# Optimization experiments

Hardware: AMD Instinct MI355X
Metric: run time of the kernel (lower is better)

The kernel has to match this reference:

```python
import jax, jax.numpy as jnp
import numpy as np

EPS = 1e-10


def setup_inputs() -> dict:
    key = jax.random.key(0)
    k1, k2 = jax.random.split(key)
    x = jax.random.normal(k1, (64, 512, 256), dtype=jnp.float32)          # (N, code_dim, T)
    codebooks = jax.random.normal(k2, (6, 1024, 512), dtype=jnp.float32)  # (Q, nb_code, code_dim)
    return {"x": x, "codebooks": codebooks}


def _quantize_layer(x_flat, cb):
    # x_flat: (NT, D), cb: (C, D)
    dist = (jnp.sum(x_flat * x_flat, axis=-1, keepdims=True)
            - 2.0 * (x_flat @ cb.T)
            + jnp.sum(cb * cb, axis=-1))          # (NT, C)
    idx = jnp.argmin(dist, axis=-1)               # (NT,)
    x_d = cb[idx]                                 # gather, (NT, D)
    return idx, x_d


def reference(x, codebooks):
    N, D, T = x.shape
    Q, C, _ = codebooks.shape
    NT = N * T

    residual = x
    quantized_out = jnp.zeros_like(x)
    all_indices, losses, perps = [], [], []

    for q in range(Q):  # fixed small number of sequential quantizer stages
        cb = codebooks[q]
        # preprocess: (N, D, T) -> (NT, D)
        x_flat = residual.transpose(0, 2, 1).reshape(NT, D)
        idx, x_d = _quantize_layer(x_flat, cb)

        # commitment loss (codebook side detached; EMA-trained codebook)
        commit_loss = jnp.mean((x_flat - jax.lax.stop_gradient(x_d)) ** 2)

        # perplexity of code usage
        probs = jnp.zeros((C,), dtype=x.dtype).at[idx].add(1.0) / NT
        perplexity = jnp.exp(-jnp.sum(probs * jnp.log(probs + EPS)))

        # straight-through estimator, back to (N, D, T)
        quantized = x_flat + jax.lax.stop_gradient(x_d - x_flat)
        quantized = quantized.reshape(N, T, D).transpose(0, 2, 1)

        residual = residual - jax.lax.stop_gradient(quantized)
        quantized_out = quantized_out + quantized

        all_indices.append(idx.reshape(N, T))
        losses.append(commit_loss)
        perps.append(perplexity)

    all_indices = jnp.stack(all_indices, axis=-1)      # (N, T, Q)
    mean_loss = sum(losses) / Q
    mean_perplexity = sum(perps) / Q
    return quantized_out, all_indices, mean_loss, mean_perplexity
```

## Files before the change

### kernel.cpp

```cpp
#include <hip/hip_runtime.h>
#include <hip/hip_fp16.h>
#include <hip/hip_bf16.h>
#include <stdint.h>


#define NTROWS 16384
#define DDIM   512
#define CCODES 1024
#define QSTAGE 6

#define OFF_R      ((size_t)0)
#define OFF_RBF    ((size_t)33554432)
#define OFF_CBBF   ((size_t)50331648)
#define OFF_CAND   ((size_t)56623104)
#define OFF_CBSQ   ((size_t)58720256)
#define OFF_HIST   ((size_t)58744832)
#define OFF_LOSS   ((size_t)58769408)
#define WS_END     ((size_t)58775552)

#define OUT_IDX_OFF  ((size_t)8388608)
#define OUT_SCAL_OFF ((size_t)8486912)

typedef __attribute__((ext_vector_type(8))) short short8;
typedef __attribute__((ext_vector_type(8))) unsigned short ushort8v;
typedef __attribute__((ext_vector_type(4))) float f32x4;

__device__ __forceinline__ unsigned short f2bf(float f) {
    uint32_t u = __float_as_uint(f);
    uint32_t r = (u + 0x7fffu + ((u >> 16) & 1u)) >> 16;
    return (unsigned short)r;
}
__device__ __forceinline__ uint32_t fkey(float f) {
    uint32_t u = __float_as_uint(f);
    return u ^ ((uint32_t)((int32_t)u >> 31) | 0x80000000u);
}
__device__ __forceinline__ float funkey(uint32_t k) {
    uint32_t u = (k & 0x80000000u) ? (k ^ 0x80000000u) : ~k;
    return __uint_as_float(u);
}
__device__ __forceinline__ uint32_t umin32(uint32_t a, uint32_t b) { return a < b ? a : b; }
__device__ __forceinline__ uint32_t umax32(uint32_t a, uint32_t b) { return a > b ? a : b; }
__device__ __forceinline__ float wave_sum(float v) {
    for (int m = 32; m; m >>= 1) v += __shfl_xor(v, m, 64);
    return v;
}
__device__ __forceinline__ uint32_t wave_min_u32(uint32_t v) {
    for (int m = 32; m; m >>= 1) v = umin32(v, (uint32_t)__shfl_xor((int)v, m, 64));
    return v;
}
__device__ __forceinline__ void async_load16(const void* g, void* l) {
    __builtin_amdgcn_global_load_lds(
        (__attribute__((address_space(1))) void*)(void*)g,
        (__attribute__((address_space(3))) void*)l, 16, 0, 0);
}

__global__ __launch_bounds__(256) void prep_kernel(
    const float* __restrict__ x, const float* __restrict__ cb,
    float* __restrict__ r, unsigned short* __restrict__ rbf,
    unsigned short* __restrict__ cbbf, float* __restrict__ cbsq,
    unsigned int* __restrict__ hist, float* __restrict__ loss_bins)
{
    __shared__ float tile[32][33];
    if (blockIdx.x < 1536) {
        const int wave = threadIdx.x >> 6, lane = threadIdx.x & 63;
        const int row = blockIdx.x * 4 + wave;
        const float* p = cb + (size_t)row * DDIM;
        unsigned short* pb = cbbf + (size_t)row * DDIM;
        float s = 0.f;
#pragma unroll
        for (int t = 0; t < 8; ++t) {
            float v = p[lane + 64 * t];
            pb[lane + 64 * t] = f2bf(v);
            s += v * v;
        }
        s = wave_sum(s);
        if (lane == 0) cbsq[row] = s;
        if (blockIdx.x == 0) {
            for (int i = threadIdx.x; i < QSTAGE * CCODES; i += 256) hist[i] = 0u;
            for (int i = threadIdx.x; i < QSTAGE * 256; i += 256) loss_bins[i] = 0.f;
        }
    } else {
        const int bidx = blockIdx.x - 1536;
        const int d0 = (bidx & 15) * 32;
        const int t0 = ((bidx >> 4) & 7) * 32;
        const int n  = bidx >> 7;
        const int tx = threadIdx.x & 31, ty = threadIdx.x >> 5;
        const float* xp = x + (size_t)n * (DDIM * 256);
#pragma unroll
        for (int s = 0; s < 4; ++s) {
            int dd = ty + s * 8;
            tile[dd][tx] = xp[(size_t)(d0 + dd) * 256 + t0 + tx];
        }
        __syncthreads();
#pragma unroll
        for (int s = 0; s < 4; ++s) {
            int tt = ty + s * 8;
            float v = tile[tx][tt];
            size_t off = (size_t)(n * 256 + t0 + tt) * DDIM + d0 + tx;
            r[off] = v;
            rbf[off] = f2bf(v);
        }
    }
}

#define GBK 32
__global__ __launch_bounds__(512, 2) void gemm_dist_kernel(
    const unsigned short* __restrict__ Abf,
    const unsigned short* __restrict__ Bbf,
    const float* __restrict__ cbsq,
    uint32_t* __restrict__ cand)
{
    __shared__ __align__(16) unsigned short lA[4][256][GBK];
    __shared__ __align__(16) unsigned short lB[4][256][GBK];
    const int tid = threadIdx.x;
    const int wave = tid >> 6, lane = tid & 63;
    const int quad = lane >> 4, l15 = lane & 15;
    const int tm = blockIdx.x, tn = blockIdx.y;
    const int wm = wave >> 2, wn = wave & 3;

    f32x4 acc[8][4];
#pragma unroll
    for (int i = 0; i < 8; ++i)
#pragma unroll
        for (int j = 0; j < 4; ++j) acc[i][j] = (f32x4){0.f, 0.f, 0.f, 0.f};

    const int srow = wave * 32 + (lane >> 2);
    const int gch  = (lane & 3) ^ ((lane >> 3) & 3);
    const unsigned short* gA0 = Abf + ((size_t)tm * 256 + srow) * DDIM + gch * 8;
    const unsigned short* gA1 = gA0 + 16 * DDIM;
    const unsigned short* gB0 = Bbf + ((size_t)tn * 256 + srow) * DDIM + gch * 8;
    const unsigned short* gB1 = gB0 + 16 * DDIM;
    const int dro0 = wave * 32, dro1 = wave * 32 + 16;

#pragma unroll
    for (int st = 0; st < 3; ++st) {
        const size_t ko = (size_t)st * GBK;
        async_load16(gA0 + ko, &lA[st][dro0][0] + lane * 8);
        async_load16(gA1 + ko, &lA[st][dro1][0] + lane * 8);
        async_load16(gB0 + ko, &lB[st][dro0][0] + lane * 8);
        async_load16(gB1 + ko, &lB[st][dro1][0] + lane * 8);
    }
    asm volatile("s_waitcnt vmcnt(8)" ::: "memory");
    __builtin_amdgcn_s_barrier();

    const int cq = (quad ^ ((l15 >> 1) & 3)) * 8;

#pragma unroll
    for (int kt = 0; kt < 16; ++kt) {
        const int buf = kt & 3;
        const int sb  = (kt + 3) & 3;
        const size_t ko = (size_t)(kt + 3) * GBK;

        short8 afA[4], bfr[4];
#pragma unroll
        for (int i = 0; i < 4; ++i)
            afA[i] = *(const short8*)&lA[buf][wm * 128 + i * 16 + l15][cq];
#pragma unroll
        for (int j = 0; j < 4; ++j)
            bfr[j] = *(const short8*)&lB[buf][wn * 64 + j * 16 + l15][cq];
        if (kt <= 12) {
            async_load16(gA0 + ko, &lA[sb][dro0][0] + lane * 8);
            async_load16(gA1 + ko, &lA[sb][dro1][0] + lane * 8);
        }
        __builtin_amdgcn_s_barrier();
        asm volatile("s_waitcnt lgkmcnt(0)" ::: "memory");
        __builtin_amdgcn_sched_barrier(0);
        __builtin_amdgcn_s_setprio(1);
#pragma unroll
        for (int i = 0; i < 4; ++i)
#pragma unroll
            for (int j = 0; j < 4; ++j)
                acc[i][j] = __builtin_amdgcn_mfma_f32_16x16x32_bf16(
                    afA[i], bfr[j], acc[i][j], 0, 0, 0);
        __builtin_amdgcn_s_setprio(0);
        __builtin_amdgcn_s_barrier();

        short8 afB[4];
#pragma unroll
        for (int i = 0; i < 4; ++i)
            afB[i] = *(const short8*)&lA[buf][wm * 128 + (i + 4) * 16 + l15][cq];
        if (kt <= 12) {
            async_load16(gB0 + ko, &lB[sb][dro0][0] + lane * 8);
            async_load16(gB1 + ko, &lB[sb][dro1][0] + lane * 8);
        }
        __builtin_amdgcn_s_barrier();
        asm volatile("s_waitcnt lgkmcnt(0)" ::: "memory");
        __builtin_amdgcn_sched_barrier(0);
        __builtin_amdgcn_s_setprio(1);
#pragma unroll
        for (int i = 0; i < 4; ++i)
#pragma unroll
            for (int j = 0; j < 4; ++j)
                acc[i + 4][j] = __builtin_amdgcn_mfma_f32_16x16x32_bf16(
                    afB[i], bfr[j], acc[i + 4][j], 0, 0, 0);
        __builtin_amdgcn_s_setprio(0);

        if (kt <= 12)      asm volatile("s_waitcnt vmcnt(8)" ::: "memory");
        else if (kt == 13) asm volatile("s_waitcnt vmcnt(4)" ::: "memory");
        else if (kt == 14) asm volatile("s_waitcnt vmcnt(0)" ::: "memory");
        if (kt < 15) __builtin_amdgcn_s_barrier();
    }

    const int rowq = tm * 256 + wm * 128 + quad * 4;
    const int colb = tn * 256 + wn * 64 + l15;
    const int g    = tn * 4 + wn;
    float cbs[4];
#pragma unroll
    for (int j = 0; j < 4; ++j) cbs[j] = cbsq[colb + j * 16];
#pragma unroll
    for (int i = 0; i < 8; ++i) {
#pragma unroll
        for (int reg = 0; reg < 4; ++reg) {
            const int row = rowq + i * 16 + reg;
            uint32_t k[4];
#pragma unroll
            for (int j = 0; j < 4; ++j) {
                float dv = cbs[j] - 2.0f * acc[i][j][reg];
                k[j] = (fkey(dv) & ~1023u) | (uint32_t)(colb + j * 16);
            }
            uint32_t m01 = umin32(k[0], k[1]), M01 = umax32(k[0], k[1]);
            uint32_t m23 = umin32(k[2], k[3]), M23 = umax32(k[2], k[3]);
            uint32_t k1 = umin32(m01, m23);
            uint32_t k2 = umin32(umax32(m01, m23), umin32(M01, M23));
#pragma unroll
            for (int m = 1; m < 16; m <<= 1) {
                uint32_t o1 = (uint32_t)__shfl_xor((int)k1, m, 64);
                uint32_t o2 = (uint32_t)__shfl_xor((int)k2, m, 64);
                uint32_t n1 = umin32(k1, o1);
                uint32_t n2 = umin32(umax32(k1, o1), umin32(k2, o2));
                k1 = n1; k2 = n2;
            }
            if (l15 == 0)
                *(uint2*)&cand[((size_t)row * 16 + g) * 2] = make_uint2(k1, k2);
        }
    }
}

#define MARGIN 8.0f
__global__ __launch_bounds__(256, 4) void refine_kernel(
    float* __restrict__ r, unsigned short* __restrict__ rbf,
    const float* __restrict__ cbq, const float* __restrict__ cbsqq,
    const uint32_t* __restrict__ cand,
    float* __restrict__ out_idx, unsigned int* __restrict__ histq,
    float* __restrict__ loss_bins, int q, int write_bf)
{
    const int wave = threadIdx.x >> 6, lane = threadIdx.x & 63;
    const int nt0 = (blockIdx.x * 4 + wave) * 4;

    float4 ra[4], rb[4];
    uint32_t key[4];
#pragma unroll
    for (int i = 0; i < 4; ++i) {
        const float4* r4 = (const float4*)(r + (size_t)(nt0 + i) * DDIM);
        ra[i] = r4[lane * 2];
        rb[i] = r4[lane * 2 + 1];
    }
#pragma unroll
    for (int i = 0; i < 4; ++i) {
        key[i] = 0xFFFFFFFFu;
        if (lane < 32) key[i] = cand[(size_t)(nt0 + i) * 32 + lane];
    }

    uint32_t kmin[4];
#pragma unroll
    for (int i = 0; i < 4; ++i) kmin[i] = key[i];
    for (int m = 32; m; m >>= 1) {
#pragma unroll
        for (int i = 0; i < 4; ++i)
            kmin[i] = umin32(kmin[i], (uint32_t)__shfl_xor((int)kmin[i], m, 64));
    }

    float sx[4];
#pragma unroll
    for (int i = 0; i < 4; ++i)
        sx[i] = ra[i].x * ra[i].x + ra[i].y * ra[i].y + ra[i].z * ra[i].z + ra[i].w * ra[i].w
              + rb[i].x * rb[i].x + rb[i].y * rb[i].y + rb[i].z * rb[i].z + rb[i].w * rb[i].w;
    for (int m = 32; m; m >>= 1) {
#pragma unroll
        for (int i = 0; i < 4; ++i) sx[i] += __shfl_xor(sx[i], m, 64);
    }

    unsigned long long mask[4];
#pragma unroll
    for (int i = 0; i < 4; ++i) {
        const float thr = funkey(kmin[i] & ~1023u) + MARGIN;
        mask[i] = __ballot(lane < 32 && funkey(key[i] & ~1023u) <= thr);
    }

    float best[4] = {1e30f, 1e30f, 1e30f, 1e30f};
    int bestc[4] = {CCODES, CCODES, CCODES, CCODES};

    while (mask[0] | mask[1] | mask[2] | mask[3]) {
        bool act[4]; int src[4], cc[4];
#pragma unroll
        for (int i = 0; i < 4; ++i) {
            act[i] = (mask[i] != 0ull);
            src[i] = act[i] ? (__ffsll(mask[i]) - 1) : 0;
            if (act[i]) mask[i] &= mask[i] - 1;
            cc[i] = __shfl((int)(key[i] & 1023u), src[i], 64);
        }
        float4 ca[4], cbb[4];
#pragma unroll
        for (int i = 0; i < 4; ++i) {
            const float4* crow = (const float4*)(cbq + (size_t)cc[i] * DDIM);
            ca[i]  = crow[lane * 2];
            cbb[i] = crow[lane * 2 + 1];
        }
        float d[4];
#pragma unroll
        for (int i = 0; i < 4; ++i)
            d[i] = ra[i].x * ca[i].x + ra[i].y * ca[i].y + ra[i].z * ca[i].z + ra[i].w * ca[i].w
                 + rb[i].x * cbb[i].x + rb[i].y * cbb[i].y + rb[i].z * cbb[i].z + rb[i].w * cbb[i].w;
        for (int m = 32; m; m >>= 1) {
#pragma unroll
            for (int i = 0; i < 4; ++i) d[i] += __shfl_xor(d[i], m, 64);
        }
#pragma unroll
        for (int i = 0; i < 4; ++i) {
            if (act[i]) {
                const float de = (sx[i] - 2.0f * d[i]) + cbsqq[cc[i]];
                if (de < best[i] || (de == best[i] && cc[i] < bestc[i])) {
                    best[i] = de; bestc[i] = cc[i];
                }
            }
        }
    }

#pragma unroll
    for (int i = 0; i < 4; ++i) {
        const float4* cbest = (const float4*)(cbq + (size_t)bestc[i] * DDIM);
        float4 ba = cbest[lane * 2], bb = cbest[lane * 2 + 1];
        float4 na = make_float4(ra[i].x - ba.x, ra[i].y - ba.y,
                                ra[i].z - ba.z, ra[i].w - ba.w);
        float4 nb = make_float4(rb[i].x - bb.x, rb[i].y - bb.y,
                                rb[i].z - bb.z, rb[i].w - bb.w);
        float4* rw = (float4*)(r + (size_t)(nt0 + i) * DDIM);
        rw[lane * 2] = na; rw[lane * 2 + 1] = nb;
        if (write_bf) {
            ushort8v pk8;
            pk8[0] = f2bf(na.x); pk8[1] = f2bf(na.y);
            pk8[2] = f2bf(na.z); pk8[3] = f2bf(na.w);
            pk8[4] = f2bf(nb.x); pk8[5] = f2bf(nb.y);
            pk8[6] = f2bf(nb.z); pk8[7] = f2bf(nb.w);
            *(ushort8v*)(rbf + (size_t)(nt0 + i) * DDIM + lane * 8) = pk8;
        }
        if (lane == 0) {
            out_idx[(size_t)(nt0 + i) * QSTAGE + q] = (float)bestc[i];
            atomicAdd(&histq[bestc[i]], 1u);
            atomicAdd(&loss_bins[q * 256 + ((nt0 + i) & 255)], best[i]);
        }
    }
}

__global__ __launch_bounds__(256) void final_kernel(
    const float* __restrict__ x, const float* __restrict__ r,
    float* __restrict__ out,
    const unsigned int* __restrict__ hist, const float* __restrict__ loss_bins,
    float* __restrict__ out2)
{
    __shared__ float tile[32][33];
    __shared__ float red[4];
    __shared__ float perp_acc;
    const int tid = threadIdx.x, wave = tid >> 6, lane = tid & 63;

    if (blockIdx.x < 8192) {
        const int bidx = blockIdx.x;
        const int d0 = (bidx & 15) * 32;
        const int t0 = ((bidx >> 4) & 7) * 32;
        const int n  = bidx >> 7;
        const int tx = tid & 31, ty = tid >> 5;
#pragma unroll
        for (int s = 0; s < 4; ++s) {
            int tt = ty + s * 8;
            tile[tt][tx] = r[(size_t)(n * 256 + t0 + tt) * DDIM + d0 + tx];
        }
        __syncthreads();
        const float* xp = x + (size_t)n * (DDIM * 256);
        float* op = out + (size_t)n * (DDIM * 256);
#pragma unroll
        for (int s = 0; s < 4; ++s) {
            int dd = ty + s * 8;
            size_t off = (size_t)(d0 + dd) * 256 + t0 + tx;
            op[off] = xp[off] - tile[tx][dd];
        }
        return;
    }

    if (tid == 0) perp_acc = 0.f;
    __syncthreads();
    for (int q = 0; q < QSTAGE; ++q) {
        float s = 0.f;
        for (int c = tid; c < CCODES; c += 256) {
            float p = (float)hist[q * CCODES + c] * (1.0f / (float)NTROWS);
            s += p * logf(p + 1e-10f);
        }
        s = wave_sum(s);
        if (lane == 0) red[wave] = s;
        __syncthreads();
        if (tid == 0) {
            float tot = red[0] + red[1] + red[2] + red[3];
            perp_acc += expf(-tot);
        }
        __syncthreads();
    }
    float ls = 0.f;
    for (int i = tid; i < QSTAGE * 256; i += 256) ls += loss_bins[i];
    ls = wave_sum(ls);
    if (lane == 0) red[wave] = ls;
    __syncthreads();
    if (tid == 0) {
        float lsum = red[0] + red[1] + red[2] + red[3];
        out2[0] = (lsum / (float)QSTAGE) / ((float)NTROWS * (float)DDIM);
        out2[1] = perp_acc / (float)QSTAGE;
    }
}

extern "C" void kernel_launch(void* const* d_in, const int* in_sizes, int n_in,
                              void* d_out, int out_size, void* d_ws, size_t ws_size,
                              hipStream_t stream)
{
    const float* x  = (const float*)d_in[0];
    const float* cb = (const float*)d_in[1];
    float* out = (float*)d_out;
    char* ws = (char*)d_ws;

    float*          r      = (float*)(ws + OFF_R);
    unsigned short* rbf    = (unsigned short*)(ws + OFF_RBF);
    unsigned short* cbbf   = (unsigned short*)(ws + OFF_CBBF);
    uint32_t*       cand   = (uint32_t*)(ws + OFF_CAND);
    float*          cbsq   = (float*)(ws + OFF_CBSQ);
    unsigned int*   hist   = (unsigned int*)(ws + OFF_HIST);
    float*          lbins  = (float*)(ws + OFF_LOSS);

    prep_kernel<<<9728, 256, 0, stream>>>(x, cb, r, rbf, cbbf, cbsq, hist, lbins);

    for (int q = 0; q < QSTAGE; ++q) {
        const size_t cboff = (size_t)q * CCODES * DDIM;
        gemm_dist_kernel<<<dim3(64, 4), 512, 0, stream>>>(
            rbf, cbbf + cboff, cbsq + q * CCODES, cand);
        refine_kernel<<<1024, 256, 0, stream>>>(
            r, rbf, cb + cboff, cbsq + q * CCODES, cand,
            out + OUT_IDX_OFF, hist + q * CCODES, lbins,
            q, (q < QSTAGE - 1) ? 1 : 0);
    }

    final_kernel<<<8193, 256, 0, stream>>>(x, r, out, hist, lbins,
                                           out + OUT_SCAL_OFF);
}
```

Baseline: 492.5 us.

## Fuse all quantizer stages into one persistent kernel with register-resident residual

Replaces the per-stage GEMM and refine kernel pair (twelve launches) with a single kernel. Each block owns 64 rows, keeps their residual in registers across all six stages, converts it to bf16 straight into LDS, streams codebook tiles, and keeps candidates in LDS instead of global memory. This removes the global round trips for the bf16 residual, the candidate buffer and the fp32 residual between stages, along with the launch overheads. In exchange only 256 blocks of 64 rows run, so there is much less A-tile reuse: every block re-streams the full bf16 codebook for each stage, and occupancy is low.

```diff
diff --git a/kernel.cpp b/kernel.cpp
--- a/kernel.cpp
+++ b/kernel.cpp
@@ -10,13 +10,10 @@
 #define QSTAGE 6
 
 #define OFF_R      ((size_t)0)
-#define OFF_RBF    ((size_t)33554432)
 #define OFF_CBBF   ((size_t)50331648)
-#define OFF_CAND   ((size_t)56623104)
 #define OFF_CBSQ   ((size_t)58720256)
 #define OFF_HIST   ((size_t)58744832)
 #define OFF_LOSS   ((size_t)58769408)
-#define WS_END     ((size_t)58775552)
 
 #define OUT_IDX_OFF  ((size_t)8388608)
 #define OUT_SCAL_OFF ((size_t)8486912)
@@ -44,10 +41,6 @@
     for (int m = 32; m; m >>= 1) v += __shfl_xor(v, m, 64);
     return v;
 }
-__device__ __forceinline__ uint32_t wave_min_u32(uint32_t v) {
-    for (int m = 32; m; m >>= 1) v = umin32(v, (uint32_t)__shfl_xor((int)v, m, 64));
-    return v;
-}
 __device__ __forceinline__ void async_load16(const void* g, void* l) {
     __builtin_amdgcn_global_load_lds(
         (__attribute__((address_space(1))) void*)(void*)g,
@@ -56,7 +49,7 @@
 
 __global__ __launch_bounds__(256) void prep_kernel(
     const float* __restrict__ x, const float* __restrict__ cb,
-    float* __restrict__ r, unsigned short* __restrict__ rbf,
+    float* __restrict__ r,
     unsigned short* __restrict__ cbbf, float* __restrict__ cbsq,
     unsigned int* __restrict__ hist, float* __restrict__ loss_bins)
 {
@@ -95,260 +88,238 @@
 #pragma unroll
         for (int s = 0; s < 4; ++s) {
             int tt = ty + s * 8;
-            float v = tile[tx][tt];
-            size_t off = (size_t)(n * 256 + t0 + tt) * DDIM + d0 + tx;
-            r[off] = v;
-            rbf[off] = f2bf(v);
-        }
-    }
-}
-
-#define GBK 32
-__global__ __launch_bounds__(512, 2) void gemm_dist_kernel(
-    const unsigned short* __restrict__ Abf,
-    const unsigned short* __restrict__ Bbf,
+            r[(size_t)(n * 256 + t0 + tt) * DDIM + d0 + tx] = tile[tx][tt];
+        }
+    }
+}
+
+#define MARGIN 8.0f
+__global__ __launch_bounds__(512, 2) void fused_vq_kernel(
+    float* __restrict__ r,
+    const unsigned short* __restrict__ cbbf,
+    const float* __restrict__ cb,
     const float* __restrict__ cbsq,
-    uint32_t* __restrict__ cand)
+    float* __restrict__ out_idx, unsigned int* __restrict__ hist,
+    float* __restrict__ loss_bins)
 {
-    __shared__ __align__(16) unsigned short lA[4][256][GBK];
-    __shared__ __align__(16) unsigned short lB[4][256][GBK];
+    __shared__ __align__(16) unsigned short lA[16][64][32];
+    __shared__ __align__(16) unsigned short lB[2][512][32];
+    __shared__ uint32_t cand_lds[64][32];
+
     const int tid = threadIdx.x;
     const int wave = tid >> 6, lane = tid & 63;
     const int quad = lane >> 4, l15 = lane & 15;
-    const int tm = blockIdx.x, tn = blockIdx.y;
-    const int wm = wave >> 2, wn = wave & 3;
-
-    f32x4 acc[8][4];
-#pragma unroll
-    for (int i = 0; i < 8; ++i)
-#pragma unroll
-        for (int j = 0; j < 4; ++j) acc[i][j] = (f32x4){0.f, 0.f, 0.f, 0.f};
-
-    const int srow = wave * 32 + (lane >> 2);
-    const int gch  = (lane & 3) ^ ((lane >> 3) & 3);
-    const unsigned short* gA0 = Abf + ((size_t)tm * 256 + srow) * DDIM + gch * 8;
-    const unsigned short* gA1 = gA0 + 16 * DDIM;
-    const unsigned short* gB0 = Bbf + ((size_t)tn * 256 + srow) * DDIM + gch * 8;
-    const unsigned short* gB1 = gB0 + 16 * DDIM;
-    const int dro0 = wave * 32, dro1 = wave * 32 + 16;
-
-#pragma unroll
-    for (int st = 0; st < 3; ++st) {
-        const size_t ko = (size_t)st * GBK;
-        async_load16(gA0 + ko, &lA[st][dro0][0] + lane * 8);
-        async_load16(gA1 + ko, &lA[st][dro1][0] + lane * 8);
-        async_load16(gB0 + ko, &lB[st][dro0][0] + lane * 8);
-        async_load16(gB1 + ko, &lB[st][dro1][0] + lane * 8);
-    }
-    asm volatile("s_waitcnt vmcnt(8)" ::: "memory");
-    __builtin_amdgcn_s_barrier();
-
-    const int cq = (quad ^ ((l15 >> 1) & 3)) * 8;
-
-#pragma unroll
-    for (int kt = 0; kt < 16; ++kt) {
-        const int buf = kt & 3;
-        const int sb  = (kt + 3) & 3;
-        const size_t ko = (size_t)(kt + 3) * GBK;
-
-        short8 afA[4], bfr[4];
-#pragma unroll
-        for (int i = 0; i < 4; ++i)
-            afA[i] = *(const short8*)&lA[buf][wm * 128 + i * 16 + l15][cq];
-#pragma unroll
-        for (int j = 0; j < 4; ++j)
-            bfr[j] = *(const short8*)&lB[buf][wn * 64 + j * 16 + l15][cq];
-        if (kt <= 12) {
-            async_load16(gA0 + ko, &lA[sb][dro0][0] + lane * 8);
-            async_load16(gA1 + ko, &lA[sb][dro1][0] + lane * 8);
-        }
-        __builtin_amdgcn_s_barrier();
-        asm volatile("s_waitcnt lgkmcnt(0)" ::: "memory");
-        __builtin_amdgcn_sched_barrier(0);
-        __builtin_amdgcn_s_setprio(1);
-#pragma unroll
-        for (int i = 0; i < 4; ++i)
-#pragma unroll
-            for (int j = 0; j < 4; ++j)
-                acc[i][j] = __builtin_amdgcn_mfma_f32_16x16x32_bf16(
-                    afA[i], bfr[j], acc[i][j], 0, 0, 0);
-        __builtin_amdgcn_s_setprio(0);
-        __builtin_amdgcn_s_barrier();
-
-        short8 afB[4];
-#pragma unroll
-        for (int i = 0; i < 4; ++i)
-            afB[i] = *(const short8*)&lA[buf][wm * 128 + (i + 4) * 16 + l15][cq];
-        if (kt <= 12) {
-            async_load16(gB0 + ko, &lB[sb][dro0][0] + lane * 8);
-            async_load16(gB1 + ko, &lB[sb][dro1][0] + lane * 8);
-        }
-        __builtin_amdgcn_s_barrier();
-        asm volatile("s_waitcnt lgkmcnt(0)" ::: "memory");
-        __builtin_amdgcn_sched_barrier(0);
-        __builtin_amdgcn_s_setprio(1);
-#pragma unroll
-        for (int i = 0; i < 4; ++i)
-#pragma unroll
-            for (int j = 0; j < 4; ++j)
-                acc[i + 4][j] = __builtin_amdgcn_mfma_f32_16x16x32_bf16(
-                    afB[i], bfr[j], acc[i + 4][j], 0, 0, 0);
-        __builtin_amdgcn_s_setprio(0);
-
-        if (kt <= 12)      asm volatile("s_waitcnt vmcnt(8)" ::: "memory");
-        else if (kt == 13) asm volatile("s_waitcnt vmcnt(4)" ::: "memory");
-        else if (kt == 14) asm volatile("s_waitcnt vmcnt(0)" ::: "memory");
-        if (kt < 15) __builtin_amdgcn_s_barrier();
-    }
-
-    const int rowq = tm * 256 + wm * 128 + quad * 4;
-    const int colb = tn * 256 + wn * 64 + l15;
-    const int g    = tn * 4 + wn;
-    float cbs[4];
-#pragma unroll
-    for (int j = 0; j < 4; ++j) cbs[j] = cbsq[colb + j * 16];
-#pragma unroll
-    for (int i = 0; i < 8; ++i) {
-#pragma unroll
-        for (int reg = 0; reg < 4; ++reg) {
-            const int row = rowq + i * 16 + reg;
-            uint32_t k[4];
-#pragma unroll
-            for (int j = 0; j < 4; ++j) {
-                float dv = cbs[j] - 2.0f * acc[i][j][reg];
-                k[j] = (fkey(dv) & ~1023u) | (uint32_t)(colb + j * 16);
-            }
-            uint32_t m01 = umin32(k[0], k[1]), M01 = umax32(k[0], k[1]);
-            uint32_t m23 = umin32(k[2], k[3]), M23 = umax32(k[2], k[3]);
-            uint32_t k1 = umin32(m01, m23);
-            uint32_t k2 = umin32(umax32(m01, m23), umin32(M01, M23));
-#pragma unroll
-            for (int m = 1; m < 16; m <<= 1) {
-                uint32_t o1 = (uint32_t)__shfl_xor((int)k1, m, 64);
-                uint32_t o2 = (uint32_t)__shfl_xor((int)k2, m, 64);
-                uint32_t n1 = umin32(k1, o1);
-                uint32_t n2 = umin32(umax32(k1, o1), umin32(k2, o2));
-                k1 = n1; k2 = n2;
-            }
-            if (l15 == 0)
-                *(uint2*)&cand[((size_t)row * 16 + g) * 2] = make_uint2(k1, k2);
-        }
-    }
-}
-
-#define MARGIN 8.0f
-__global__ __launch_bounds__(256, 4) void refine_kernel(
-    float* __restrict__ r, unsigned short* __restrict__ rbf,
-    const float* __restrict__ cbq, const float* __restrict__ cbsqq,
-    const uint32_t* __restrict__ cand,
-    float* __restrict__ out_idx, unsigned int* __restrict__ histq,
-    float* __restrict__ loss_bins, int q, int write_bf)
-{
-    const int wave = threadIdx.x >> 6, lane = threadIdx.x & 63;
-    const int nt0 = (blockIdx.x * 4 + wave) * 4;
-
-    float4 ra[4], rb[4];
-    uint32_t key[4];
-#pragma unroll
-    for (int i = 0; i < 4; ++i) {
-        const float4* r4 = (const float4*)(r + (size_t)(nt0 + i) * DDIM);
-        ra[i] = r4[lane * 2];
-        rb[i] = r4[lane * 2 + 1];
-    }
-#pragma unroll
-    for (int i = 0; i < 4; ++i) {
-        key[i] = 0xFFFFFFFFu;
-        if (lane < 32) key[i] = cand[(size_t)(nt0 + i) * 32 + lane];
-    }
-
-    uint32_t kmin[4];
-#pragma unroll
-    for (int i = 0; i < 4; ++i) kmin[i] = key[i];
-    for (int m = 32; m; m >>= 1) {
-#pragma unroll
-        for (int i = 0; i < 4; ++i)
-            kmin[i] = umin32(kmin[i], (uint32_t)__shfl_xor((int)kmin[i], m, 64));
-    }
-
-    float sx[4];
-#pragma unroll
-    for (int i = 0; i < 4; ++i)
-        sx[i] = ra[i].x * ra[i].x + ra[i].y * ra[i].y + ra[i].z * ra[i].z + ra[i].w * ra[i].w
-              + rb[i].x * rb[i].x + rb[i].y * rb[i].y + rb[i].z * rb[i].z + rb[i].w * rb[i].w;
-    for (int m = 32; m; m >>= 1) {
-#pragma unroll
-        for (int i = 0; i < 4; ++i) sx[i] += __shfl_xor(sx[i], m, 64);
-    }
-
-    unsigned long long mask[4];
-#pragma unroll
-    for (int i = 0; i < 4; ++i) {
-        const float thr = funkey(kmin[i] & ~1023u) + MARGIN;
-        mask[i] = __ballot(lane < 32 && funkey(key[i] & ~1023u) <= thr);
-    }
-
-    float best[4] = {1e30f, 1e30f, 1e30f, 1e30f};
-    int bestc[4] = {CCODES, CCODES, CCODES, CCODES};
-
-    while (mask[0] | mask[1] | mask[2] | mask[3]) {
-        bool act[4]; int src[4], cc[4];
-#pragma unroll
-        for (int i = 0; i < 4; ++i) {
-            act[i] = (mask[i] != 0ull);
-            src[i] = act[i] ? (__ffsll(mask[i]) - 1) : 0;
-            if (act[i]) mask[i] &= mask[i] - 1;
-            cc[i] = __shfl((int)(key[i] & 1023u), src[i], 64);
-        }
-        float4 ca[4], cbb[4];
-#pragma unroll
-        for (int i = 0; i < 4; ++i) {
-            const float4* crow = (const float4*)(cbq + (size_t)cc[i] * DDIM);
-            ca[i]  = crow[lane * 2];
-            cbb[i] = crow[lane * 2 + 1];
-        }
-        float d[4];
-#pragma unroll
-        for (int i = 0; i < 4; ++i)
-            d[i] = ra[i].x * ca[i].x + ra[i].y * ca[i].y + ra[i].z * ca[i].z + ra[i].w * ca[i].w
-                 + rb[i].x * cbb[i].x + rb[i].y * cbb[i].y + rb[i].z * cbb[i].z + rb[i].w * cbb[i].w;
-        for (int m = 32; m; m >>= 1) {
-#pragma unroll
-            for (int i = 0; i < 4; ++i) d[i] += __shfl_xor(d[i], m, 64);
-        }
-#pragma unroll
-        for (int i = 0; i < 4; ++i) {
-            if (act[i]) {
-                const float de = (sx[i] - 2.0f * d[i]) + cbsqq[cc[i]];
-                if (de < best[i] || (de == best[i] && cc[i] < bestc[i])) {
-                    best[i] = de; bestc[i] = cc[i];
-                }
-            }
-        }
-    }
-
-#pragma unroll
-    for (int i = 0; i < 4; ++i) {
-        const float4* cbest = (const float4*)(cbq + (size_t)bestc[i] * DDIM);
-        float4 ba = cbest[lane * 2], bb = cbest[lane * 2 + 1];
-        float4 na = make_float4(ra[i].x - ba.x, ra[i].y - ba.y,
-                                ra[i].z - ba.z, ra[i].w - ba.w);
-        float4 nb = make_float4(rb[i].x - bb.x, rb[i].y - bb.y,
-                                rb[i].z - bb.z, rb[i].w - bb.w);
-        float4* rw = (float4*)(r + (size_t)(nt0 + i) * DDIM);
-        rw[lane * 2] = na; rw[lane * 2 + 1] = nb;
-        if (write_bf) {
-            ushort8v pk8;
-            pk8[0] = f2bf(na.x); pk8[1] = f2bf(na.y);
-            pk8[2] = f2bf(na.z); pk8[3] = f2bf(na.w);
-            pk8[4] = f2bf(nb.x); pk8[5] = f2bf(nb.y);
-            pk8[6] = f2bf(nb.z); pk8[7] = f2bf(nb.w);
-            *(ushort8v*)(rbf + (size_t)(nt0 + i) * DDIM + lane * 8) = pk8;
-        }
-        if (lane == 0) {
-            out_idx[(size_t)(nt0 + i) * QSTAGE + q] = (float)bestc[i];
-            atomicAdd(&histq[bestc[i]], 1u);
-            atomicAdd(&loss_bins[q * 256 + ((nt0 + i) & 255)], best[i]);
-        }
+    const int nt_base = blockIdx.x * 64;
+
+    float4 rA[8], rB[8];
+#pragma unroll
+    for (int rr = 0; rr < 8; ++rr) {
+        const float* rp = r + (size_t)(nt_base + wave * 8 + rr) * DDIM + lane * 8;
+        rA[rr] = *(const float4*)rp;
+        rB[rr] = *(const float4*)(rp + 4);
+    }
+
+    const int gch = (lane & 3) ^ ((lane >> 3) & 3);
+    const int cq  = (quad ^ ((l15 >> 1) & 3)) * 8;
+
+    for (int q = 0; q < QSTAGE; ++q) {
+        const unsigned short* cbbf_q = cbbf + (size_t)q * CCODES * DDIM;
+        const float* cb_q   = cb   + (size_t)q * CCODES * DDIM;
+        const float* cbsq_q = cbsq + q * CCODES;
+
+#pragma unroll
+        for (int rr = 0; rr < 8; ++rr) {
+            const int rl = wave * 8 + rr;
+            ushort8v pk;
+            pk[0] = f2bf(rA[rr].x); pk[1] = f2bf(rA[rr].y);
+            pk[2] = f2bf(rA[rr].z); pk[3] = f2bf(rA[rr].w);
+            pk[4] = f2bf(rB[rr].x); pk[5] = f2bf(rB[rr].y);
+            pk[6] = f2bf(rB[rr].z); pk[7] = f2bf(rB[rr].w);
+            *(ushort8v*)&lA[lane >> 2][rl][((lane & 3) ^ ((rl >> 1) & 3)) * 8] = pk;
+        }
+        __syncthreads();
+
+#pragma unroll
+        for (int ch = 0; ch < 2; ++ch) {
+            f32x4 acc[4][4];
+#pragma unroll
+            for (int i = 0; i < 4; ++i)
+#pragma unroll
+                for (int j = 0; j < 4; ++j) acc[i][j] = (f32x4){0.f, 0.f, 0.f, 0.f};
+
+            {
+                const unsigned short* src = cbbf_q +
+                    ((size_t)ch * 512 + wave * 64 + (lane >> 2)) * DDIM + gch * 8;
+                unsigned short* dst = &lB[0][wave * 64][0] + lane * 8;
+#pragma unroll
+                for (int t = 0; t < 4; ++t)
+                    async_load16(src + (size_t)t * 16 * DDIM, dst + t * 16 * 32);
+            }
+#pragma unroll
+            for (int kt = 0; kt < 16; ++kt) {
+                if (kt < 15) {
+                    const unsigned short* src = cbbf_q +
+                        ((size_t)ch * 512 + wave * 64 + (lane >> 2)) * DDIM +
+                        (size_t)(kt + 1) * 32 + gch * 8;
+                    unsigned short* dst = &lB[(kt + 1) & 1][wave * 64][0] + lane * 8;
+#pragma unroll
+                    for (int t = 0; t < 4; ++t)
+                        async_load16(src + (size_t)t * 16 * DDIM, dst + t * 16 * 32);
+                }
+                if (kt < 15) asm volatile("s_waitcnt vmcnt(4)" ::: "memory");
+                else         asm volatile("s_waitcnt vmcnt(0)" ::: "memory");
+                __builtin_amdgcn_s_barrier();
+                __builtin_amdgcn_sched_barrier(0);
+
+                short8 af[4], bfr[4];
+#pragma unroll
+                for (int i = 0; i < 4; ++i)
+                    af[i] = *(const short8*)&lA[kt][i * 16 + l15][cq];
+#pragma unroll
+                for (int j = 0; j < 4; ++j)
+                    bfr[j] = *(const short8*)&lB[kt & 1][wave * 64 + j * 16 + l15][cq];
+
+                __builtin_amdgcn_s_setprio(1);
+#pragma unroll
+                for (int i = 0; i < 4; ++i)
+#pragma unroll
+                    for (int j = 0; j < 4; ++j)
+                        acc[i][j] = __builtin_amdgcn_mfma_f32_16x16x32_bf16(
+                            af[i], bfr[j], acc[i][j], 0, 0, 0);
+                __builtin_amdgcn_s_setprio(0);
+                __builtin_amdgcn_s_barrier();
+            }
+
+            const int colb = ch * 512 + wave * 64 + l15;
+            const int g    = ch * 8 + wave;
+            float cbs[4];
+#pragma unroll
+            for (int j = 0; j < 4; ++j) cbs[j] = cbsq_q[colb + j * 16];
+#pragma unroll
+            for (int i = 0; i < 4; ++i) {
+#pragma unroll
+                for (int reg = 0; reg < 4; ++reg) {
+                    uint32_t k[4];
+#pragma unroll
+                    for (int j = 0; j < 4; ++j) {
+                        float dv = cbs[j] - 2.0f * acc[i][j][reg];
+                        k[j] = (fkey(dv) & ~1023u) | (uint32_t)(colb + j * 16);
+                    }
+                    uint32_t m01 = umin32(k[0], k[1]), M01 = umax32(k[0], k[1]);
+                    uint32_t m23 = umin32(k[2], k[3]), M23 = umax32(k[2], k[3]);
+                    uint32_t k1 = umin32(m01, m23);
+                    uint32_t k2 = umin32(umax32(m01, m23), umin32(M01, M23));
+#pragma unroll
+                    for (int m = 1; m < 16; m <<= 1) {
+                        uint32_t o1 = (uint32_t)__shfl_xor((int)k1, m, 64);
+                        uint32_t o2 = (uint32_t)__shfl_xor((int)k2, m, 64);
+                        uint32_t n1 = umin32(k1, o1);
+                        uint32_t n2 = umin32(umax32(k1, o1), umin32(k2, o2));
+                        k1 = n1; k2 = n2;
+                    }
+                    if (l15 == 0)
+                        *(uint2*)&cand_lds[i * 16 + quad * 4 + reg][g * 2] =
+                            make_uint2(k1, k2);
+                }
+            }
+        }
+        __syncthreads();
+
+#pragma unroll
+        for (int b2 = 0; b2 < 2; ++b2) {
+            const int lr0 = wave * 8 + b2 * 4;
+            uint32_t key[4], kmin[4];
+            float sx[4];
+#pragma unroll
+            for (int i = 0; i < 4; ++i) {
+                key[i] = 0xFFFFFFFFu;
+                if (lane < 32) key[i] = cand_lds[lr0 + i][lane];
+                kmin[i] = key[i];
+            }
+            for (int m = 32; m; m >>= 1) {
+#pragma unroll
+                for (int i = 0; i < 4; ++i)
+                    kmin[i] = umin32(kmin[i], (uint32_t)__shfl_xor((int)kmin[i], m, 64));
+            }
+#pragma unroll
+            for (int i = 0; i < 4; ++i) {
+                const float4 a = rA[b2 * 4 + i], c = rB[b2 * 4 + i];
+                sx[i] = a.x * a.x + a.y * a.y + a.z * a.z + a.w * a.w
+                      + c.x * c.x + c.y * c.y + c.z * c.z + c.w * c.w;
+            }
+            for (int m = 32; m; m >>= 1) {
+#pragma unroll
+                for (int i = 0; i < 4; ++i) sx[i] += __shfl_xor(sx[i], m, 64);
+            }
+            unsigned long long mask[4];
+#pragma unroll
+            for (int i = 0; i < 4; ++i) {
+                const float thr = funkey(kmin[i] & ~1023u) + MARGIN;
+                mask[i] = __ballot(lane < 32 && funkey(key[i] & ~1023u) <= thr);
+            }
+            float best[4] = {1e30f, 1e30f, 1e30f, 1e30f};
+            int bestc[4] = {CCODES, CCODES, CCODES, CCODES};
+            while (mask[0] | mask[1] | mask[2] | mask[3]) {
+                bool act[4]; int src[4], cc[4];
+#pragma unroll
+                for (int i = 0; i < 4; ++i) {
+                    act[i] = (mask[i] != 0ull);
+                    src[i] = act[i] ? (__ffsll(mask[i]) - 1) : 0;
+                    if (act[i]) mask[i] &= mask[i] - 1;
+                    cc[i] = __shfl((int)(key[i] & 1023u), src[i], 64);
+                }
+                float4 ca[4], cbb[4];
+#pragma unroll
+                for (int i = 0; i < 4; ++i) {
+                    const float4* crow = (const float4*)(cb_q + (size_t)cc[i] * DDIM);
+                    ca[i]  = crow[lane * 2];
+                    cbb[i] = crow[lane * 2 + 1];
+                }
+                float d[4];
+#pragma unroll
+                for (int i = 0; i < 4; ++i) {
+                    const float4 a = rA[b2 * 4 + i], c2 = rB[b2 * 4 + i];
+                    d[i] = a.x * ca[i].x + a.y * ca[i].y + a.z * ca[i].z + a.w * ca[i].w
+                         + c2.x * cbb[i].x + c2.y * cbb[i].y + c2.z * cbb[i].z + c2.w * cbb[i].w;
+                }
+                for (int m = 32; m; m >>= 1) {
+#pragma unroll
+                    for (int i = 0; i < 4; ++i) d[i] += __shfl_xor(d[i], m, 64);
+                }
+#pragma unroll
+                for (int i = 0; i < 4; ++i) {
+                    if (act[i]) {
+                        const float de = (sx[i] - 2.0f * d[i]) + cbsq_q[cc[i]];
+                        if (de < best[i] || (de == best[i] && cc[i] < bestc[i])) {
+                            best[i] = de; bestc[i] = cc[i];
+                        }
+                    }
+                }
+            }
+#pragma unroll
+            for (int i = 0; i < 4; ++i) {
+                const float4* cbest = (const float4*)(cb_q + (size_t)bestc[i] * DDIM);
+                float4 ba = cbest[lane * 2], bb = cbest[lane * 2 + 1];
+                rA[b2 * 4 + i].x -= ba.x; rA[b2 * 4 + i].y -= ba.y;
+                rA[b2 * 4 + i].z -= ba.z; rA[b2 * 4 + i].w -= ba.w;
+                rB[b2 * 4 + i].x -= bb.x; rB[b2 * 4 + i].y -= bb.y;
+                rB[b2 * 4 + i].z -= bb.z; rB[b2 * 4 + i].w -= bb.w;
+                if (lane == 0) {
+                    const int nt = nt_base + lr0 + i;
+                    out_idx[(size_t)nt * QSTAGE + q] = (float)bestc[i];
+                    atomicAdd(&hist[q * CCODES + bestc[i]], 1u);
+                    atomicAdd(&loss_bins[q * 256 + (nt & 255)], best[i]);
+                }
+            }
+        }
+        __syncthreads();
+    }
+
+#pragma unroll
+    for (int rr = 0; rr < 8; ++rr) {
+        float* rp = r + (size_t)(nt_base + wave * 8 + rr) * DDIM + lane * 8;
+        *(float4*)rp = rA[rr];
+        *(float4*)(rp + 4) = rB[rr];
     }
 }
 
@@ -425,24 +396,15 @@
     char* ws = (char*)d_ws;
 
     float*          r      = (float*)(ws + OFF_R);
-    unsigned short* rbf    = (unsigned short*)(ws + OFF_RBF);
     unsigned short* cbbf   = (unsigned short*)(ws + OFF_CBBF);
-    uint32_t*       cand   = (uint32_t*)(ws + OFF_CAND);
     float*          cbsq   = (float*)(ws + OFF_CBSQ);
     unsigned int*   hist   = (unsigned int*)(ws + OFF_HIST);
     float*          lbins  = (float*)(ws + OFF_LOSS);
 
-    prep_kernel<<<9728, 256, 0, stream>>>(x, cb, r, rbf, cbbf, cbsq, hist, lbins);
-
-    for (int q = 0; q < QSTAGE; ++q) {
-        const size_t cboff = (size_t)q * CCODES * DDIM;
-        gemm_dist_kernel<<<dim3(64, 4), 512, 0, stream>>>(
-            rbf, cbbf + cboff, cbsq + q * CCODES, cand);
-        refine_kernel<<<1024, 256, 0, stream>>>(
-            r, rbf, cb + cboff, cbsq + q * CCODES, cand,
-            out + OUT_IDX_OFF, hist + q * CCODES, lbins,
-            q, (q < QSTAGE - 1) ? 1 : 0);
-    }
+    prep_kernel<<<9728, 256, 0, stream>>>(x, cb, r, cbbf, cbsq, hist, lbins);
+
+    fused_vq_kernel<<<256, 512, 0, stream>>>(
+        r, cbbf, cb, cbsq, out + OUT_IDX_OFF, hist, lbins);
 
     final_kernel<<<8193, 256, 0, stream>>>(x, r, out, hist, lbins,
                                            out + OUT_SCAL_OFF);
```

New measurement: 426.0 us. 1.16x faster.
